# Performance work log

Hardware: AMD Instinct MI355X
Metric: run time of the kernel (lower is better)

Reference implementation:

```python
import jax, jax.numpy as jnp
import numpy as np

B, T, C = 4, 2048, 1024
H = 16
D = C // H  # head_dim = 64


def setup_inputs() -> dict:
    key = jax.random.key(0)
    ks = jax.random.split(key, 6)
    s = 1.0 / np.sqrt(C)
    x = jax.random.normal(ks[0], (B, T, C), dtype=jnp.float32)
    Wq = jax.random.normal(ks[1], (C, C), dtype=jnp.float32) * s
    Wk = jax.random.normal(ks[2], (C, C), dtype=jnp.float32) * s
    Wv = jax.random.normal(ks[3], (C, C), dtype=jnp.float32) * s
    Wo = jax.random.normal(ks[4], (C, C), dtype=jnp.float32) * s
    bo = jnp.zeros((C,), dtype=jnp.float32)
    # causal mask, 1 = attend, 0 = masked (masked_fill(mask==0, -inf))
    mask = jnp.broadcast_to(jnp.tril(jnp.ones((T, T), dtype=jnp.int32)), (B, T, T))
    return {"x": x, "mask": mask, "Wq": Wq, "Wk": Wk, "Wv": Wv, "Wo": Wo, "bo": bo}


def reference(x, mask, Wq, Wk, Wv, Wo, bo):
    Bx, Tx, Cx = x.shape
    # projections; nn.Linear computes x @ W.T, here W is stored as (C, C) applied as x @ W
    Q = (x @ Wq).reshape(Bx, Tx, H, D).transpose(0, 2, 1, 3)  # (B,H,T,D)
    K = (x @ Wk).reshape(Bx, Tx, H, D).transpose(0, 2, 1, 3)
    V = (x @ Wv).reshape(Bx, Tx, H, D).transpose(0, 2, 1, 3)
    scores = jnp.einsum('bhqd,bhkd->bhqk', Q, K) / jnp.sqrt(jnp.float32(D))
    scores = jnp.where(mask[:, None, :, :] == 0, -jnp.inf, scores)
    attn = jax.nn.softmax(scores, axis=-1)
    ctx = jnp.einsum('bhqk,bhkd->bhqd', attn, V)  # (B,H,T,D)
    ctx = ctx.transpose(0, 2, 1, 3).reshape(Bx, Tx, Cx)
    return ctx @ Wo + bo
```

## Files before the change

### kernel.cpp

```cpp
#include <hip/hip_runtime.h>
#include <hip/hip_bf16.h>


#define B_  4
#define T_  2048
#define C_  1024
#define H_  16
#define D_  64
#define M_  (B_*T_)

#define LOG2E 1.4426950408889634f

using bf16x8 = __attribute__((ext_vector_type(8))) short;
using f32x4  = __attribute__((ext_vector_type(4))) float;
using u16x4  = __attribute__((ext_vector_type(4))) unsigned short;

__device__ __forceinline__ unsigned short f2bf(float f) {
  union { float f; unsigned u; } cv; cv.f = f;
  unsigned u = cv.u;
  u += 0x7fffu + ((u >> 16) & 1u);
  return (unsigned short)(u >> 16);
}

__device__ __forceinline__ unsigned cvt_pk_bf16(float lo, float hi) {
  unsigned r;
  asm("v_cvt_pk_bf16_f32 %0, %1, %2" : "=v"(r) : "v"(lo), "v"(hi));
  return r;
}

__device__ __forceinline__ float exp2fast(float x) {
#if __has_builtin(__builtin_amdgcn_exp2f)
  return __builtin_amdgcn_exp2f(x);
#else
  return exp2f(x);
#endif
}

__device__ __forceinline__ void lds_load16(void* lds, const void* g) {
  __builtin_amdgcn_global_load_lds(
      (const __attribute__((address_space(1))) unsigned int*)g,
      (__attribute__((address_space(3))) unsigned int*)lds,
      16, 0, 0);
}

__global__ __launch_bounds__(256) void conv_x_kernel(
    const float* __restrict__ x, unsigned short* __restrict__ xb) {
  int i = blockIdx.x * 256 + threadIdx.x;
  const float4* xv = (const float4*)x;
  float4 a = xv[i * 2 + 0];
  float4 b = xv[i * 2 + 1];
  using u16x8 = __attribute__((ext_vector_type(8))) unsigned short;
  u16x8 o;
  o[0]=f2bf(a.x); o[1]=f2bf(a.y); o[2]=f2bf(a.z); o[3]=f2bf(a.w);
  o[4]=f2bf(b.x); o[5]=f2bf(b.y); o[6]=f2bf(b.z); o[7]=f2bf(b.w);
  *(u16x8*)&xb[(size_t)i * 8] = o;
}

__global__ __launch_bounds__(256) void conv_wt_kernel(
    const float* __restrict__ W0, const float* __restrict__ W1,
    const float* __restrict__ W2, const float* __restrict__ W3,
    unsigned short* __restrict__ WT) {
  __shared__ float tile[64][65];
  const float* W = (blockIdx.z == 0) ? W0 : (blockIdx.z == 1) ? W1
                 : (blockIdx.z == 2) ? W2 : W3;
  unsigned short* o = WT + (size_t)blockIdx.z * C_ * C_;
  const int k0 = blockIdx.y * 64, n0 = blockIdx.x * 64;
  const int tr = threadIdx.x >> 6;
  const int tc = threadIdx.x & 63;
#pragma unroll
  for (int i = 0; i < 16; ++i) {
    int k = tr + i * 4;
    tile[k][tc] = W[(size_t)(k0 + k) * C_ + n0 + tc];
  }
  __syncthreads();
#pragma unroll
  for (int i = 0; i < 16; ++i) {
    int n = tr + i * 4;
    o[(size_t)(n0 + n) * C_ + k0 + tc] = f2bf(tile[tc][n]);
  }
}

template <int EPI>
__global__ __launch_bounds__(256) void gemm128(
    const unsigned short* __restrict__ A, const unsigned short* __restrict__ BT,
    void* __restrict__ out, const float* __restrict__ bias, int K) {
  __shared__ unsigned short As[128][32];
  __shared__ unsigned short Bs[128][32];

  const int tid  = threadIdx.x;
  const int wid  = tid >> 6, lane = tid & 63;
  const int wr   = wid >> 1, wc = wid & 1;
  const int fr   = lane & 15, fq = lane >> 4;
  const int bm   = blockIdx.y, bn = blockIdx.x;

  const unsigned short* aP = A  + (size_t)(bm * 128 + wid * 32 + (lane >> 2)) * K + (lane & 3) * 8;
  const unsigned short* bP = BT + (size_t)(bn * 128 + wid * 32 + (lane >> 2)) * K + (lane & 3) * 8;
  unsigned short* asB = &As[wid * 32][0];
  unsigned short* bsB = &Bs[wid * 32][0];

  f32x4 acc[4][4] = {};

  for (int k0 = 0; k0 < K; k0 += 32) {
    lds_load16(asB,           aP + k0);
    lds_load16(asB + 16 * 32, aP + (size_t)16 * K + k0);
    lds_load16(bsB,           bP + k0);
    lds_load16(bsB + 16 * 32, bP + (size_t)16 * K + k0);
    __syncthreads();

    bf16x8 af[4], bfr[4];
#pragma unroll
    for (int mi = 0; mi < 4; ++mi)
      af[mi] = *(const bf16x8*)&As[wr * 64 + mi * 16 + fr][fq * 8];
#pragma unroll
    for (int ni = 0; ni < 4; ++ni)
      bfr[ni] = *(const bf16x8*)&Bs[wc * 64 + ni * 16 + fr][fq * 8];
#pragma unroll
    for (int mi = 0; mi < 4; ++mi)
#pragma unroll
      for (int ni = 0; ni < 4; ++ni)
        acc[mi][ni] = __builtin_amdgcn_mfma_f32_16x16x32_bf16(
            af[mi], bfr[ni], acc[mi][ni], 0, 0, 0);
    __syncthreads();
  }

  if (EPI == 0) {
    unsigned short* o = (unsigned short*)out;
#pragma unroll
    for (int mi = 0; mi < 4; ++mi) {
      int m  = bm * 128 + wr * 64 + mi * 16 + fq * 4;
      int b  = m >> 11;
      int t0 = m & 2047;
#pragma unroll
      for (int ni = 0; ni < 4; ++ni) {
        int n = bn * 128 + wc * 64 + ni * 16 + fr;
        int mat = n >> 10;
        int nc  = n & 1023;
        int h = nc >> 6, d = nc & 63;
        float sc_ = (mat == 0) ? (0.125f * LOG2E) : 1.0f;
        size_t base = (size_t)mat * ((size_t)M_ * C_) + ((size_t)(b * H_ + h) << 17) + d;
#pragma unroll
        for (int r = 0; r < 4; ++r)
          o[base + (size_t)(t0 + r) * D_] = f2bf(acc[mi][ni][r] * sc_);
      }
    }
  } else {
    float* o = (float*)out;
#pragma unroll
    for (int mi = 0; mi < 4; ++mi) {
      int m = bm * 128 + wr * 64 + mi * 16 + fq * 4;
#pragma unroll
      for (int ni = 0; ni < 4; ++ni) {
        int n = bn * 128 + wc * 64 + ni * 16 + fr;
        float bv = bias[n];
#pragma unroll
        for (int r = 0; r < 4; ++r)
          o[(size_t)(m + r) * C_ + n] = acc[mi][ni][r] + bv;
      }
    }
  }
}

#define KSTR 72
__global__ __launch_bounds__(256) void attn_kernel(
    const unsigned short* __restrict__ Qg, const unsigned short* __restrict__ Kg,
    const unsigned short* __restrict__ Vg, unsigned short* __restrict__ ctx) {
  __shared__ __align__(16) unsigned short Ks[64][KSTR];
  __shared__ __align__(16) unsigned short VTs[64][KSTR];

  const int tid = threadIdx.x, wid = tid >> 6, lane = tid & 63;
  const int fr = lane & 15, fq = lane >> 4;

  const int bid = blockIdx.x;
  const int xcd = bid & 7, j = bid >> 3;
  const int bh = xcd * 8 + (j & 7);
  const int qt = 15 - (j >> 3);
  const int b = bh >> 4, h = bh & 15;
  const size_t base = (size_t)bh * (T_ * D_);

  const int ksr = tid >> 2, ksc = tid & 3;
  const int kpr = ((ksr >> 5) & 1) * 32 + ((ksr >> 2) & 1) * 16 +
                  ((ksr >> 3) & 3) * 4 + (ksr & 3);
  const unsigned short* Kptr = Kg + base + (size_t)ksr * D_ + ksc * 8;
  const int vc = tid >> 5, vr_ = tid & 31;
  const unsigned short* Vptr = Vg + base + (size_t)(2 * vr_) * D_ + vc * 8;

  int4 kr0, kr1, va, vb;
  auto stage_load = [&](int kv) {
    const unsigned short* kp = Kptr + (size_t)kv * D_;
    kr0 = *(const int4*)kp;
    kr1 = *(const int4*)(kp + 32);
    const unsigned short* vp = Vptr + (size_t)kv * D_;
    va = *(const int4*)vp;
    vb = *(const int4*)(vp + D_);
  };
  auto stage_write = [&]() {
    *(int4*)&Ks[kpr][ksc * 8]       = kr0;
    *(int4*)&Ks[kpr][(ksc + 4) * 8] = kr1;
    const unsigned short* pa = (const unsigned short*)&va;
    const unsigned short* pb = (const unsigned short*)&vb;
#pragma unroll
    for (int i = 0; i < 8; ++i) {
      unsigned w = (unsigned)pa[i] | ((unsigned)pb[i] << 16);
      *(unsigned*)&VTs[vc * 8 + i][2 * vr_] = w;
    }
  };

  stage_load(0);
  stage_write();

  const int qbase = qt * 128;

  bf16x8 qf[2][2];
#pragma unroll
  for (int x = 0; x < 2; ++x)
#pragma unroll
    for (int t = 0; t < 2; ++t)
      qf[x][t] = *(const bf16x8*)
          &Qg[base + (size_t)(qbase + 64 * x + wid * 16 + fr) * D_ + t * 32 + fq * 8];

  f32x4 acc[2][4] = {};
  float m_run[2] = {-__builtin_inff(), -__builtin_inff()};
  float l_run[2] = {0.f, 0.f};

  const int nsteps = 2 * qt + 2;
  int kv0 = 0;
  for (int s = 0; s < nsteps; ++s) {
    const bool have_next = (s + 1 < nsteps);

    __syncthreads();
    if (have_next) stage_load(kv0 + 64);

    bf16x8 kf[8];
#pragma unroll
    for (int nt = 0; nt < 4; ++nt)
#pragma unroll
      for (int t = 0; t < 2; ++t)
        kf[nt * 2 + t] = *(const bf16x8*)&Ks[nt * 16 + fr][t * 32 + fq * 8];

    bf16x8 pf[2][2];
#pragma unroll
    for (int x = 0; x < 2; ++x) {
      f32x4 sv[4];
      __builtin_amdgcn_s_setprio(1);
#pragma unroll
      for (int nt = 0; nt < 4; ++nt) {
        f32x4 sa = {};
        sa = __builtin_amdgcn_mfma_f32_16x16x32_bf16(kf[nt * 2 + 0], qf[x][0], sa, 0, 0, 0);
        sa = __builtin_amdgcn_mfma_f32_16x16x32_bf16(kf[nt * 2 + 1], qf[x][1], sa, 0, 0, 0);
        sv[nt] = sa;
      }
      __builtin_amdgcn_s_setprio(0);

      float mt = -__builtin_inff();
      if (kv0 >= qbase + 64 * x) {
        const int qi = qbase + 64 * x + wid * 16 + fr;
#pragma unroll
        for (int nt = 0; nt < 4; ++nt)
#pragma unroll
          for (int r = 0; r < 4; ++r) {
            int kvi = kv0 + 32 * (nt >> 1) + 8 * fq + 4 * (nt & 1) + r;
            float v = sv[nt][r];
            if (kvi > qi) v = -__builtin_inff();
            sv[nt][r] = v;
            mt = fmaxf(mt, v);
          }
      } else {
#pragma unroll
        for (int nt = 0; nt < 4; ++nt)
#pragma unroll
          for (int r = 0; r < 4; ++r) mt = fmaxf(mt, sv[nt][r]);
      }
      mt = fmaxf(mt, __shfl_xor(mt, 16));
      mt = fmaxf(mt, __shfl_xor(mt, 32));

      {
        float mn = fmaxf(m_run[x], mt);
        float c  = (mn == m_run[x]) ? 1.0f : exp2fast(m_run[x] - mn);
        m_run[x] = mn;
#pragma unroll
        for (int dt = 0; dt < 4; ++dt) acc[x][dt] *= c;
        l_run[x] *= c;
      }

      float lsum = 0.f;
      int pw[8];
#pragma unroll
      for (int nt = 0; nt < 4; ++nt) {
        float p0 = exp2fast(sv[nt][0] - m_run[x]);
        float p1 = exp2fast(sv[nt][1] - m_run[x]);
        float p2 = exp2fast(sv[nt][2] - m_run[x]);
        float p3 = exp2fast(sv[nt][3] - m_run[x]);
        lsum += (p0 + p1) + (p2 + p3);
        pw[(nt >> 1) * 4 + (nt & 1) * 2 + 0] = (int)cvt_pk_bf16(p0, p1);
        pw[(nt >> 1) * 4 + (nt & 1) * 2 + 1] = (int)cvt_pk_bf16(p2, p3);
      }
      lsum += __shfl_xor(lsum, 16);
      lsum += __shfl_xor(lsum, 32);
      l_run[x] += lsum;

#pragma unroll
      for (int t = 0; t < 2; ++t) {
        int4 v4 = {pw[t * 4 + 0], pw[t * 4 + 1], pw[t * 4 + 2], pw[t * 4 + 3]};
        pf[x][t] = __builtin_bit_cast(bf16x8, v4);
      }
    }

    __builtin_amdgcn_s_setprio(1);
#pragma unroll
    for (int t = 0; t < 2; ++t)
#pragma unroll
      for (int dt = 0; dt < 4; ++dt) {
        bf16x8 vf = *(const bf16x8*)&VTs[dt * 16 + fr][t * 32 + fq * 8];
        acc[0][dt] = __builtin_amdgcn_mfma_f32_16x16x32_bf16(vf, pf[0][t], acc[0][dt], 0, 0, 0);
        acc[1][dt] = __builtin_amdgcn_mfma_f32_16x16x32_bf16(vf, pf[1][t], acc[1][dt], 0, 0, 0);
      }
    __builtin_amdgcn_s_setprio(0);

    __syncthreads();
    if (have_next) stage_write();

    kv0 += 64;
  }

#pragma unroll
  for (int x = 0; x < 2; ++x) {
    float linv = 1.0f / l_run[x];
    unsigned short* orow =
        ctx + (size_t)(b * T_ + qbase + 64 * x + wid * 16 + fr) * C_ + h * D_;
#pragma unroll
    for (int dt = 0; dt < 4; ++dt) {
      u16x4 o;
#pragma unroll
      for (int r = 0; r < 4; ++r) o[r] = f2bf(acc[x][dt][r] * linv);
      *(u16x4*)&orow[dt * 16 + fq * 4] = o;
    }
  }
}

extern "C" void kernel_launch(void* const* d_in, const int* in_sizes, int n_in,
                              void* d_out, int out_size, void* d_ws, size_t ws_size,
                              hipStream_t stream) {
  const float* x  = (const float*)d_in[0];
  const float* Wq = (const float*)d_in[2];
  const float* Wk = (const float*)d_in[3];
  const float* Wv = (const float*)d_in[4];
  const float* Wo = (const float*)d_in[5];
  const float* bo = (const float*)d_in[6];

  unsigned short* xb  = (unsigned short*)d_ws;
  unsigned short* wqt = xb  + (size_t)M_ * C_;
  unsigned short* wot = wqt + (size_t)3 * C_ * C_;
  unsigned short* Qb  = wot + (size_t)C_ * C_;
  unsigned short* ctxb = xb;

  conv_x_kernel<<<4096, 256, 0, stream>>>(x, xb);
  conv_wt_kernel<<<dim3(16, 16, 4), 256, 0, stream>>>(Wq, Wk, Wv, Wo, wqt);

  gemm128<0><<<dim3(24, M_ / 128), 256, 0, stream>>>(xb, wqt, Qb, nullptr, C_);

  attn_kernel<<<dim3(1024), 256, 0, stream>>>(
      Qb, Qb + (size_t)M_ * C_, Qb + (size_t)2 * M_ * C_, ctxb);

  gemm128<1><<<dim3(8, M_ / 128), 256, 0, stream>>>(ctxb, wot, d_out, bo, C_);
}
```

Baseline: 199.2 us.

## Double-buffer attention K/V tiles, add lazy softmax rescale, XCD-aware GEMM block swizzle

The attention kernel now keeps two LDS buffers for K and V^T. The next tile is written into the other buffer, which removes the second __syncthreads per KV step. The online-softmax rescale is skipped unless some lane's new max exceeds the running max by more than 8 in log2 space. Skipping it saves exp and multiply work, but the unnormalised accumulator can grow by up to 2^8, which costs some precision in exchange. The GEMM remaps block IDs so that consecutive blocks on the same XCD share A row tiles, aiming at better L2 reuse; the remapping assumes a fixed grid shape.

```diff
diff --git a/kernel.cpp b/kernel.cpp
--- a/kernel.cpp
+++ b/kernel.cpp
@@ -91,7 +91,10 @@
   const int wid  = tid >> 6, lane = tid & 63;
   const int wr   = wid >> 1, wc = wid & 1;
   const int fr   = lane & 15, fq = lane >> 4;
-  const int bm   = blockIdx.y, bn = blockIdx.x;
+  const int bid  = blockIdx.y * gridDim.x + blockIdx.x;
+  const int xcd  = bid & 7, ii = bid >> 3;
+  const int bm   = xcd + 8 * (ii & 7);
+  const int bn   = ii >> 3;
 
   const unsigned short* aP = A  + (size_t)(bm * 128 + wid * 32 + (lane >> 2)) * K + (lane & 3) * 8;
   const unsigned short* bP = BT + (size_t)(bn * 128 + wid * 32 + (lane >> 2)) * K + (lane & 3) * 8;
@@ -164,8 +167,8 @@
 __global__ __launch_bounds__(256) void attn_kernel(
     const unsigned short* __restrict__ Qg, const unsigned short* __restrict__ Kg,
     const unsigned short* __restrict__ Vg, unsigned short* __restrict__ ctx) {
-  __shared__ __align__(16) unsigned short Ks[64][KSTR];
-  __shared__ __align__(16) unsigned short VTs[64][KSTR];
+  __shared__ __align__(16) unsigned short Ks[2][64][KSTR];
+  __shared__ __align__(16) unsigned short VTs[2][64][KSTR];
 
   const int tid = threadIdx.x, wid = tid >> 6, lane = tid & 63;
   const int fr = lane & 15, fq = lane >> 4;
@@ -193,20 +196,20 @@
     va = *(const int4*)vp;
     vb = *(const int4*)(vp + D_);
   };
-  auto stage_write = [&]() {
-    *(int4*)&Ks[kpr][ksc * 8]       = kr0;
-    *(int4*)&Ks[kpr][(ksc + 4) * 8] = kr1;
+  auto stage_write = [&](int nb) {
+    *(int4*)&Ks[nb][kpr][ksc * 8]       = kr0;
+    *(int4*)&Ks[nb][kpr][(ksc + 4) * 8] = kr1;
     const unsigned short* pa = (const unsigned short*)&va;
     const unsigned short* pb = (const unsigned short*)&vb;
 #pragma unroll
     for (int i = 0; i < 8; ++i) {
       unsigned w = (unsigned)pa[i] | ((unsigned)pb[i] << 16);
-      *(unsigned*)&VTs[vc * 8 + i][2 * vr_] = w;
+      *(unsigned*)&VTs[nb][vc * 8 + i][2 * vr_] = w;
     }
   };
 
   stage_load(0);
-  stage_write();
+  stage_write(0);
 
   const int qbase = qt * 128;
 
@@ -225,6 +228,7 @@
   const int nsteps = 2 * qt + 2;
   int kv0 = 0;
   for (int s = 0; s < nsteps; ++s) {
+    const int  cur = s & 1;
     const bool have_next = (s + 1 < nsteps);
 
     __syncthreads();
@@ -235,7 +239,7 @@
     for (int nt = 0; nt < 4; ++nt)
 #pragma unroll
       for (int t = 0; t < 2; ++t)
-        kf[nt * 2 + t] = *(const bf16x8*)&Ks[nt * 16 + fr][t * 32 + fq * 8];
+        kf[nt * 2 + t] = *(const bf16x8*)&Ks[cur][nt * 16 + fr][t * 32 + fq * 8];
 
     bf16x8 pf[2][2];
 #pragma unroll
@@ -267,15 +271,15 @@
       } else {
 #pragma unroll
         for (int nt = 0; nt < 4; ++nt)
-#pragma unroll
-          for (int r = 0; r < 4; ++r) mt = fmaxf(mt, sv[nt][r]);
+          mt = fmaxf(mt, fmaxf(fmaxf(sv[nt][0], sv[nt][1]),
+                               fmaxf(sv[nt][2], sv[nt][3])));
       }
       mt = fmaxf(mt, __shfl_xor(mt, 16));
       mt = fmaxf(mt, __shfl_xor(mt, 32));
 
-      {
+      if (__any(mt > m_run[x] + 8.0f)) {
         float mn = fmaxf(m_run[x], mt);
-        float c  = (mn == m_run[x]) ? 1.0f : exp2fast(m_run[x] - mn);
+        float c  = exp2fast(m_run[x] - mn);
         m_run[x] = mn;
 #pragma unroll
         for (int dt = 0; dt < 4; ++dt) acc[x][dt] *= c;
@@ -310,15 +314,13 @@
     for (int t = 0; t < 2; ++t)
 #pragma unroll
       for (int dt = 0; dt < 4; ++dt) {
-        bf16x8 vf = *(const bf16x8*)&VTs[dt * 16 + fr][t * 32 + fq * 8];
+        bf16x8 vf = *(const bf16x8*)&VTs[cur][dt * 16 + fr][t * 32 + fq * 8];
         acc[0][dt] = __builtin_amdgcn_mfma_f32_16x16x32_bf16(vf, pf[0][t], acc[0][dt], 0, 0, 0);
         acc[1][dt] = __builtin_amdgcn_mfma_f32_16x16x32_bf16(vf, pf[1][t], acc[1][dt], 0, 0, 0);
       }
     __builtin_amdgcn_s_setprio(0);
 
-    __syncthreads();
-    if (have_next) stage_write();
-
+    if (have_next) stage_write(cur ^ 1);
     kv0 += 64;
   }
 
```

After: 191.1 us. 1.04x faster.
